# Optimization experiments

Hardware: AMD Instinct MI355X
Metric: run time of the kernel (lower is better)

## Reference

```python
import jax, jax.numpy as jnp
import numpy as np

NUM_HEADS = 16
HIDDEN = 1024
HEAD_DIM = HIDDEN // NUM_HEADS
B, L = 1, 2048


def setup_inputs() -> dict:
    key = jax.random.key(0)
    ks = jax.random.split(key, 5)
    scale = 1.0 / np.sqrt(HIDDEN)
    x = jax.random.normal(ks[0], (B, L, HIDDEN), dtype=jnp.float32)
    Wq = jax.random.normal(ks[1], (HIDDEN, HIDDEN), dtype=jnp.float32) * scale
    Wk = jax.random.normal(ks[2], (HIDDEN, HIDDEN), dtype=jnp.float32) * scale
    Wv = jax.random.normal(ks[3], (HIDDEN, HIDDEN), dtype=jnp.float32) * scale
    Wo = jax.random.normal(ks[4], (HIDDEN, HIDDEN), dtype=jnp.float32) * scale
    return {"x": x, "Wq": Wq, "Wk": Wk, "Wv": Wv, "Wo": Wo}


def reference(x, Wq, Wk, Wv, Wo):
    Bx, Lx, _ = x.shape
    # nn.Linear computes x @ W.T (bias=False)
    q = (x @ Wq.T).reshape(Bx, Lx, NUM_HEADS, HEAD_DIM)
    k = (x @ Wk.T).reshape(Bx, Lx, NUM_HEADS, HEAD_DIM)
    v = (x @ Wv.T).reshape(Bx, Lx, NUM_HEADS, HEAD_DIM)
    # elu(.)+1 feature map
    q = jax.nn.elu(q) + 1.0
    k = jax.nn.elu(k) + 1.0
    # causal linear-attention state via cumsum of kv outer products
    kv = jnp.einsum('blhd,blhe->blhde', k, v)           # [B,L,H,D,D]
    kv_cumsum = jnp.cumsum(kv, axis=1)
    k_cumsum = jnp.cumsum(k, axis=1)
    out = jnp.einsum('blhd,blhde->blhe', q, kv_cumsum)   # [B,L,H,D]
    denom = jnp.clip(jnp.einsum('blhd,blhd->blh', q, k_cumsum), 1e-6, None)
    out = out / denom[..., None]
    return out.reshape(Bx, Lx, HIDDEN) @ Wo.T
```

## Files before the change

kernel.cpp:

```cpp
#include <hip/hip_runtime.h>
#include <hip/hip_bf16.h>

typedef __attribute__((ext_vector_type(8))) short short8;
typedef __attribute__((ext_vector_type(4))) float floatx4;
typedef __attribute__((ext_vector_type(8))) unsigned short ushortx8;
typedef __attribute__((ext_vector_type(4))) unsigned short ushortx4;
typedef unsigned short u16;

#define HIDDEN 1024
#define NH 16
#define HD 64
#define SEQ 2048
#define CHUNK 128
#define NCHUNK (SEQ / CHUNK)

__device__ __forceinline__ u16 f2bf(float f) {
    union { float f; unsigned u; } v; v.f = f;
    unsigned r = v.u + 0x7fffu + ((v.u >> 16) & 1u);
    return (u16)(r >> 16);
}
__device__ __forceinline__ float bf2f(u16 u) {
    union { unsigned u; float f; } v; v.u = ((unsigned)u) << 16;
    return v.f;
}

__device__ __forceinline__ void gl_lds16(const u16* g, u16* l) {
    __builtin_amdgcn_global_load_lds(
        (const __attribute__((address_space(1))) void*)g,
        (__attribute__((address_space(3))) void*)l,
        16, 0, 0);
}

__global__ __launch_bounds__(256)
void convert_all(const float* __restrict__ x,  const float* __restrict__ Wq,
                 const float* __restrict__ Wk, const float* __restrict__ Wv,
                 const float* __restrict__ Wo,
                 u16* __restrict__ xb, u16* __restrict__ Wb, u16* __restrict__ Wob)
{
    const int total4 = 1572864;
    for (int idx = blockIdx.x * 256 + threadIdx.x; idx < total4; idx += gridDim.x * 256) {
        const float4* src; u16* dst; int off;
        if (idx < 524288)       { src = (const float4*)x;  dst = xb;            off = idx; }
        else if (idx < 786432)  { src = (const float4*)Wq; dst = Wb;            off = idx - 524288; }
        else if (idx < 1048576) { src = (const float4*)Wk; dst = Wb + 1048576;  off = idx - 786432; }
        else if (idx < 1310720) { src = (const float4*)Wv; dst = Wb + 2097152;  off = idx - 1048576; }
        else                    { src = (const float4*)Wo; dst = Wob;           off = idx - 1310720; }
        float4 v = src[off];
        ushortx4 u = { f2bf(v.x), f2bf(v.y), f2bf(v.z), f2bf(v.w) };
        *(ushortx4*)(dst + (size_t)off * 4) = u;
    }
}

__global__ __launch_bounds__(256, 3)
void qkv_gemm64(const u16* __restrict__ A, const u16* __restrict__ Bm,
                u16* __restrict__ qkb, u16* __restrict__ kT_b, u16* __restrict__ vT_b)
{
    __shared__ u16 As[2][64 * 64];
    __shared__ u16 Bs[2][128 * 64];
    const int n0 = blockIdx.x * 128, m0 = blockIdx.y * 64;
    const int t = threadIdx.x;
    const int lane = t & 63, wave = t >> 6;
    const int ln = lane & 15, q4 = lane >> 4;
    const int wm = (wave >> 1) * 32, wn = (wave & 1) * 64;
    const int r_in = t >> 3;
    const int csw = (((t & 7) ^ (r_in & 7)) << 3);

    const u16* Ag = A + (size_t)(m0 + r_in) * 1024 + csw;
    const u16* Bg = Bm + (size_t)(n0 + r_in) * 1024 + csw;

    floatx4 acc[2][4];
#pragma unroll
    for (int i = 0; i < 2; i++)
#pragma unroll
        for (int j = 0; j < 4; j++) acc[i][j] = (floatx4)0.0f;

    auto stage = [&](int buf, int k) {
        const int k0 = k * 64;
        gl_lds16(Ag + k0, &As[buf][t * 8]);
        gl_lds16(Ag + k0 + 32 * 1024, &As[buf][2048 + t * 8]);
#pragma unroll
        for (int i = 0; i < 4; i++)
            gl_lds16(Bg + k0 + (size_t)i * 32 * 1024, &Bs[buf][i * 2048 + t * 8]);
    };
    auto compute = [&](int buf) {
#pragma unroll
        for (int s = 0; s < 2; s++) {
            const int rc = (((s * 4 + q4) ^ (ln & 7)) << 3);
            short8 af[2], bfr[4];
#pragma unroll
            for (int i = 0; i < 2; i++)
                af[i] = *(const short8*)&As[buf][(wm + i * 16 + ln) * 64 + rc];
#pragma unroll
            for (int j = 0; j < 4; j++)
                bfr[j] = *(const short8*)&Bs[buf][(wn + j * 16 + ln) * 64 + rc];
#pragma unroll
            for (int i = 0; i < 2; i++)
#pragma unroll
                for (int j = 0; j < 4; j++)
                    acc[i][j] = __builtin_amdgcn_mfma_f32_16x16x32_bf16(af[i], bfr[j], acc[i][j], 0, 0, 0);
        }
    };

    stage(0, 0);
    stage(1, 1);
    for (int i = 0; i < 14; i++) {
        asm volatile("s_waitcnt vmcnt(6)" ::: "memory");
        __builtin_amdgcn_sched_barrier(0);
        __builtin_amdgcn_s_barrier();
        compute(i & 1);
        __builtin_amdgcn_sched_barrier(0);
        __builtin_amdgcn_s_barrier();
        stage(i & 1, i + 2);
    }
    asm volatile("s_waitcnt vmcnt(6)" ::: "memory");
    __builtin_amdgcn_sched_barrier(0);
    __builtin_amdgcn_s_barrier();
    compute(0);
    asm volatile("s_waitcnt vmcnt(0)" ::: "memory");
    __builtin_amdgcn_sched_barrier(0);
    __builtin_amdgcn_s_barrier();
    compute(1);

    const int grp = n0 >> 10;
#pragma unroll
    for (int i = 0; i < 2; i++)
#pragma unroll
        for (int j = 0; j < 4; j++) {
            const int mb = m0 + wm + i * 16 + q4 * 4;
            const int n = n0 + wn + j * 16 + ln;
            const int nh = n & 1023, h = nh >> 6, e = nh & 63;
            float vals[4];
#pragma unroll
            for (int r = 0; r < 4; r++) {
                float v = acc[i][j][r];
                if (grp < 2) v = (v > 0.f) ? (v + 1.f) : __expf(v);
                vals[r] = v;
            }
            if (grp == 0) {
#pragma unroll
                for (int r = 0; r < 4; r++) qkb[(size_t)(mb + r) * 2048 + nh] = f2bf(vals[r]);
            } else if (grp == 1) {
#pragma unroll
                for (int r = 0; r < 4; r++) qkb[(size_t)(mb + r) * 2048 + 1024 + nh] = f2bf(vals[r]);
                ushortx4 u = { f2bf(vals[0]), f2bf(vals[1]), f2bf(vals[2]), f2bf(vals[3]) };
                *(ushortx4*)&kT_b[(size_t)(h * 64 + e) * 2048 + mb] = u;
            } else {
                ushortx4 u = { f2bf(vals[0]), f2bf(vals[1]), f2bf(vals[2]), f2bf(vals[3]) };
                *(ushortx4*)&vT_b[(size_t)(h * 64 + e) * 2048 + mb] = u;
            }
        }
}

__global__ __launch_bounds__(256, 2)
void chunk_stats2(const u16* __restrict__ kT_b, const u16* __restrict__ vT_b,
                  float* __restrict__ S_ws, float* __restrict__ ksum_ws)
{
    __shared__ u16 kT_l[64 * 128];
    __shared__ u16 vT_l[64 * 128];
    const int c = blockIdx.x, h = blockIdx.y;
    const int t = threadIdx.x;
    const int lane = t & 63, w = t >> 6;
    const int ln = lane & 15, q4 = lane >> 4;
#pragma unroll
    for (int i = 0; i < 4; i++) {
        const int d0 = w * 16 + i * 4 + (lane >> 4);
        const int cc = lane & 15;
        const size_t gsrc = (size_t)(h * 64 + d0) * 2048 + c * 128 + ((cc ^ (d0 & 7)) << 3);
        gl_lds16(kT_b + gsrc, &kT_l[(w * 16 + i * 4) * 128 + lane * 8]);
        gl_lds16(vT_b + gsrc, &vT_l[(w * 16 + i * 4) * 128 + lane * 8]);
    }
    __syncthreads();
    floatx4 sacc[4];
#pragma unroll
    for (int j = 0; j < 4; j++) sacc[j] = (floatx4)0.0f;
#pragma unroll
    for (int ks = 0; ks < 4; ks++) {
        const int rc = (((ks * 4 + q4) ^ (ln & 7)) << 3);
        short8 af = *(const short8*)&kT_l[(w * 16 + ln) * 128 + rc];
#pragma unroll
        for (int j = 0; j < 4; j++) {
            short8 bfr = *(const short8*)&vT_l[(j * 16 + ln) * 128 + rc];
            sacc[j] = __builtin_amdgcn_mfma_f32_16x16x32_bf16(af, bfr, sacc[j], 0, 0, 0);
        }
    }
    float* Sp = S_ws + ((size_t)(h * NCHUNK + c) << 12);
#pragma unroll
    for (int j = 0; j < 4; j++)
#pragma unroll
        for (int r = 0; r < 4; r++) {
            int d = w * 16 + q4 * 4 + r;
            int e = j * 16 + ln;
            Sp[e * 64 + d] = sacc[j][r];
        }
    if (t < 64) {
        float s = 0.f;
#pragma unroll
        for (int cc = 0; cc < 16; cc++) {
            ushortx8 v8 = *(const ushortx8*)&kT_l[t * 128 + cc * 8];
#pragma unroll
            for (int jj = 0; jj < 8; jj++) s += bf2f(v8[jj]);
        }
        ksum_ws[(h * NCHUNK + c) * 64 + t] = s;
    }
}

__global__ __launch_bounds__(256)
void scan_kv(const float* __restrict__ S_ws, const float* __restrict__ ksum_ws,
             u16* __restrict__ kvpref_b, float* __restrict__ kspref)
{
    const int h = blockIdx.x, qt = blockIdx.y;
    const int t = threadIdx.x;
    const int li = qt * 1024 + t * 4;
    const int e = li >> 6, d0 = li & 63;
    const int slot = e * 64 + ((((d0 >> 3) ^ (e & 7)) << 3) | (d0 & 7));
    float a0 = 0.f, a1 = 0.f, a2 = 0.f, a3 = 0.f;
    for (int c = 0; c < 16; c++) {
        ushortx4 u = { f2bf(a0), f2bf(a1), f2bf(a2), f2bf(a3) };
        *(ushortx4*)&kvpref_b[(((size_t)(h * 16 + c)) << 12) + slot] = u;
        float4 s4 = *(const float4*)(S_ws + (((size_t)(h * 16 + c)) << 12) + li);
        a0 += s4.x; a1 += s4.y; a2 += s4.z; a3 += s4.w;
    }
    if (qt == 0 && t < 64) {
        float a = 0.f;
        for (int c = 0; c < 16; c++) {
            kspref[(h * 16 + c) * 64 + t] = a;
            a += ksum_ws[(h * 16 + c) * 64 + t];
        }
    }
}

__global__ __launch_bounds__(512, 2)
void attn_out2(const u16* __restrict__ qkb, const u16* __restrict__ vT_b,
               const u16* __restrict__ kvpref_b, const float* __restrict__ kspref,
               u16* __restrict__ attnb)
{
    __shared__ __align__(16) u16 smem[29824];
    u16* q_l   = smem;
    u16* k_l   = smem + 8192;
    u16* kvT_l = smem + 16384;
    u16* vT_l  = smem + 20480;
    u16* P_l   = smem;
    float* kpref  = (float*)(smem + 28672);
    float* denom4 = kpref + 64;

    const int c = blockIdx.x, h = blockIdx.y;
    const int t = threadIdx.x;
    const int lane = t & 63, w = t >> 6;
    const int ln = lane & 15, q4 = lane >> 4;

    {
        const int row = t >> 3, cc = t & 7;
        const size_t gq = (size_t)(c * CHUNK + row) * 2048 + h * 64
                        + (size_t)((cc ^ (row & 7)) << 3);
        gl_lds16(qkb + gq,        &q_l[t * 8]);
        gl_lds16(qkb + gq + 1024, &k_l[t * 8]);
        const int row2 = row + 64;
        const size_t gq2 = (size_t)(c * CHUNK + row2) * 2048 + h * 64
                         + (size_t)((cc ^ (row2 & 7)) << 3);
        gl_lds16(qkb + gq2,        &q_l[4096 + t * 8]);
        gl_lds16(qkb + gq2 + 1024, &k_l[4096 + t * 8]);
        const int d = t >> 4, cv = t & 15;
        gl_lds16(vT_b + (size_t)(h * 64 + d) * 2048 + c * 128 + ((cv ^ (d & 7)) << 3),
                 &vT_l[t * 8]);
        const int d2 = d + 32;
        gl_lds16(vT_b + (size_t)(h * 64 + d2) * 2048 + c * 128 + ((cv ^ (d2 & 7)) << 3),
                 &vT_l[4096 + t * 8]);
        gl_lds16(kvpref_b + (((size_t)(h * 16 + c)) << 12) + t * 8, &kvT_l[t * 8]);
    }
    if (t < 64) kpref[t] = kspref[(h * 16 + c) * 64 + t];
    __syncthreads();

    const int pm = (w >> 2) * 64, pn = (w & 3) * 32;
    floatx4 pacc[4][2];
#pragma unroll
    for (int i = 0; i < 4; i++)
#pragma unroll
        for (int j = 0; j < 2; j++) pacc[i][j] = (floatx4)0.0f;
#pragma unroll
    for (int s = 0; s < 2; s++) {
        const int rc = (((s * 4 + q4) ^ (ln & 7)) << 3);
        short8 af[4], bfr[2];
#pragma unroll
        for (int i = 0; i < 4; i++)
            af[i] = *(const short8*)&q_l[(pm + i * 16 + ln) * 64 + rc];
#pragma unroll
        for (int j = 0; j < 2; j++)
            bfr[j] = *(const short8*)&k_l[(pn + j * 16 + ln) * 64 + rc];
#pragma unroll
        for (int i = 0; i < 4; i++)
#pragma unroll
            for (int j = 0; j < 2; j++)
                pacc[i][j] = __builtin_amdgcn_mfma_f32_16x16x32_bf16(af[i], bfr[j], pacc[i][j], 0, 0, 0);
    }
#pragma unroll
    for (int i = 0; i < 4; i++)
#pragma unroll
        for (int r = 0; r < 4; r++) {
            int rowi = pm + i * 16 + q4 * 4 + r;
            float rs = 0.f;
#pragma unroll
            for (int j = 0; j < 2; j++) {
                int col = pn + j * 16 + ln;
                float p = pacc[i][j][r];
                if (col > rowi) p = 0.f;
                pacc[i][j][r] = p;
                rs += p;
            }
#pragma unroll
            for (int off = 1; off < 16; off <<= 1) rs += __shfl_xor(rs, off, 64);
            if (ln == 0) denom4[(w & 3) * 128 + rowi] = rs;
        }
    const int ob = w * 16;
    floatx4 oacc[4];
#pragma unroll
    for (int j = 0; j < 4; j++) oacc[j] = (floatx4)0.0f;
#pragma unroll
    for (int s = 0; s < 2; s++) {
        const int rc = (((s * 4 + q4) ^ (ln & 7)) << 3);
        short8 af = *(const short8*)&q_l[(ob + ln) * 64 + rc];
#pragma unroll
        for (int j = 0; j < 4; j++) {
            short8 bfr = *(const short8*)&kvT_l[(j * 16 + ln) * 64 + rc];
            oacc[j] = __builtin_amdgcn_mfma_f32_16x16x32_bf16(af, bfr, oacc[j], 0, 0, 0);
        }
    }
    __syncthreads();
    if (t < 128) {
        float s = 0.f;
#pragma unroll
        for (int c8 = 0; c8 < 8; c8++) {
            ushortx8 v8 = *(const ushortx8*)&q_l[t * 64 + ((c8 ^ (t & 7)) << 3)];
#pragma unroll
            for (int jj = 0; jj < 8; jj++) s += bf2f(v8[jj]) * kpref[c8 * 8 + jj];
        }
        denom4[t] += s;
    }
    __syncthreads();
#pragma unroll
    for (int i = 0; i < 4; i++)
#pragma unroll
        for (int j = 0; j < 2; j++)
#pragma unroll
            for (int r = 0; r < 4; r++) {
                int rowi = pm + i * 16 + q4 * 4 + r;
                int col = pn + j * 16 + ln;
                P_l[rowi * 136 + col] = f2bf(pacc[i][j][r]);
            }
    __syncthreads();
    for (int ks = 0; ks <= (w >> 1); ks++) {
        short8 af = *(const short8*)&P_l[(ob + ln) * 136 + ks * 32 + q4 * 8];
        const int rc = (((ks * 4 + q4) ^ (ln & 7)) << 3);
#pragma unroll
        for (int j = 0; j < 4; j++) {
            short8 bfr = *(const short8*)&vT_l[(j * 16 + ln) * 128 + rc];
            oacc[j] = __builtin_amdgcn_mfma_f32_16x16x32_bf16(af, bfr, oacc[j], 0, 0, 0);
        }
    }
#pragma unroll
    for (int r = 0; r < 4; r++) {
        const int rowi = ob + q4 * 4 + r;
        float den = denom4[rowi] + denom4[128 + rowi] + denom4[256 + rowi] + denom4[384 + rowi];
        den = fmaxf(den, 1e-6f);
#pragma unroll
        for (int j = 0; j < 4; j++) {
            int e = j * 16 + ln;
            attnb[(size_t)(c * CHUNK + rowi) * HIDDEN + h * HD + e] = f2bf(oacc[j][r] / den);
        }
    }
}

__global__ __launch_bounds__(256, 3)
void out_gemm64(const u16* __restrict__ A, const u16* __restrict__ Bm,
                float* __restrict__ out)
{
    __shared__ u16 As[2][64 * 64];
    __shared__ u16 Bs[2][64 * 64];
    const int n0 = blockIdx.x * 64, m0 = blockIdx.y * 64;
    const int t = threadIdx.x;
    const int lane = t & 63, wave = t >> 6;
    const int ln = lane & 15, q4 = lane >> 4;
    const int wm = (wave >> 1) * 32, wn = (wave & 1) * 32;
    const int r_in = t >> 3;
    const int csw = (((t & 7) ^ (r_in & 7)) << 3);

    const u16* Ag = A + (size_t)(m0 + r_in) * 1024 + csw;
    const u16* Bg = Bm + (size_t)(n0 + r_in) * 1024 + csw;

    floatx4 acc[2][2];
#pragma unroll
    for (int i = 0; i < 2; i++)
#pragma unroll
        for (int j = 0; j < 2; j++) acc[i][j] = (floatx4)0.0f;

    auto stage = [&](int buf, int k) {
        const int k0 = k * 64;
        gl_lds16(Ag + k0, &As[buf][t * 8]);
        gl_lds16(Ag + k0 + 32 * 1024, &As[buf][2048 + t * 8]);
        gl_lds16(Bg + k0, &Bs[buf][t * 8]);
        gl_lds16(Bg + k0 + 32 * 1024, &Bs[buf][2048 + t * 8]);
    };
    auto compute = [&](int buf) {
#pragma unroll
        for (int s = 0; s < 2; s++) {
            const int rc = (((s * 4 + q4) ^ (ln & 7)) << 3);
            short8 af[2], bfr[2];
#pragma unroll
            for (int i = 0; i < 2; i++)
                af[i] = *(const short8*)&As[buf][(wm + i * 16 + ln) * 64 + rc];
#pragma unroll
            for (int j = 0; j < 2; j++)
                bfr[j] = *(const short8*)&Bs[buf][(wn + j * 16 + ln) * 64 + rc];
#pragma unroll
            for (int i = 0; i < 2; i++)
#pragma unroll
                for (int j = 0; j < 2; j++)
                    acc[i][j] = __builtin_amdgcn_mfma_f32_16x16x32_bf16(af[i], bfr[j], acc[i][j], 0, 0, 0);
        }
    };

    stage(0, 0);
    stage(1, 1);
    for (int i = 0; i < 14; i++) {
        asm volatile("s_waitcnt vmcnt(4)" ::: "memory");
        __builtin_amdgcn_sched_barrier(0);
        __builtin_amdgcn_s_barrier();
        compute(i & 1);
        __builtin_amdgcn_sched_barrier(0);
        __builtin_amdgcn_s_barrier();
        stage(i & 1, i + 2);
    }
    asm volatile("s_waitcnt vmcnt(4)" ::: "memory");
    __builtin_amdgcn_sched_barrier(0);
    __builtin_amdgcn_s_barrier();
    compute(0);
    asm volatile("s_waitcnt vmcnt(0)" ::: "memory");
    __builtin_amdgcn_sched_barrier(0);
    __builtin_amdgcn_s_barrier();
    compute(1);

#pragma unroll
    for (int i = 0; i < 2; i++)
#pragma unroll
        for (int j = 0; j < 2; j++)
#pragma unroll
            for (int r = 0; r < 4; r++) {
                int m = m0 + wm + i * 16 + q4 * 4 + r;
                int n = n0 + wn + j * 16 + ln;
                out[(size_t)m * 1024 + n] = acc[i][j][r];
            }
}

extern "C" void kernel_launch(void* const* d_in, const int* in_sizes, int n_in,
                              void* d_out, int out_size, void* d_ws, size_t ws_size,
                              hipStream_t stream)
{
    const float* x  = (const float*)d_in[0];
    const float* Wq = (const float*)d_in[1];
    const float* Wk = (const float*)d_in[2];
    const float* Wv = (const float*)d_in[3];
    const float* Wo = (const float*)d_in[4];
    float* out = (float*)d_out;

    char* ws = (char*)d_ws;
    const size_t MB = 1024 * 1024;
    u16* xb    = (u16*)(ws);
    u16* Wb    = (u16*)(ws + 4 * MB);
    u16* Wob   = (u16*)(ws + 10 * MB);
    u16* qkb   = (u16*)(ws + 12 * MB);
    u16* kT_b  = (u16*)(ws + 20 * MB);
    u16* vT_b  = (u16*)(ws + 24 * MB);
    float* S_ws    = (float*)(ws + 28 * MB);
    float* ksum_ws = (float*)(ws + 32 * MB);
    u16* attnb = (u16*)(ws + 33 * MB);
    u16* kvpref_b = (u16*)(ws + 37 * MB);
    float* kspref = (float*)(ws + 39 * MB);

    convert_all<<<2048, 256, 0, stream>>>(x, Wq, Wk, Wv, Wo, xb, Wb, Wob);
    qkv_gemm64<<<dim3(24, 32), 256, 0, stream>>>(xb, Wb, qkb, kT_b, vT_b);
    chunk_stats2<<<dim3(NCHUNK, NH), 256, 0, stream>>>(kT_b, vT_b, S_ws, ksum_ws);
    scan_kv<<<dim3(NH, 4), 256, 0, stream>>>(S_ws, ksum_ws, kvpref_b, kspref);
    attn_out2<<<dim3(NCHUNK, NH), 512, 0, stream>>>(qkb, vT_b, kvpref_b, kspref, attnb);
    out_gemm64<<<dim3(16, 32), 256, 0, stream>>>(attnb, Wob, out);
}
```

Baseline: 124.2 us.

## Stage QKV GEMM epilogue through LDS and remap block tiles for cache locality

The QKV GEMM epilogue now writes results into shared memory, one row-major and one transposed tile, and then emits 16-byte coalesced stores to qkb, kT_b and vT_b. Before, it issued scattered 2-byte and 8-byte global stores. Both GEMMs also switch to a 1D grid whose block indices are remapped into groups, presumably to spread tiles across the XCDs and improve L2 reuse of A and B tiles. This adds an extra LDS round trip and two barriers at the end of each block.

Result: slower. 127.8 us (+2.9%).

```diff
diff --git a/kernel.cpp b/kernel.cpp
--- a/kernel.cpp
+++ b/kernel.cpp
@@ -55,9 +55,17 @@
 void qkv_gemm64(const u16* __restrict__ A, const u16* __restrict__ Bm,
                 u16* __restrict__ qkb, u16* __restrict__ kT_b, u16* __restrict__ vT_b)
 {
-    __shared__ u16 As[2][64 * 64];
-    __shared__ u16 Bs[2][128 * 64];
-    const int n0 = blockIdx.x * 128, m0 = blockIdx.y * 64;
+    __shared__ __align__(16) u16 smem[24576];
+    auto As = (u16(*)[4096])smem;
+    auto Bs = (u16(*)[8192])(smem + 8192);
+    u16* Trow = smem;
+    u16* Tcol = smem + 8704;
+
+    const int L = blockIdx.x;
+    const int xc = L & 7, i5 = L >> 3;
+    const int m0 = (((xc >> 2) * 16) + (i5 & 15)) * 64;
+    const int n0 = (((xc & 3) * 6) + (i5 >> 4)) * 128;
+
     const int t = threadIdx.x;
     const int lane = t & 63, wave = t >> 6;
     const int ln = lane & 15, q4 = lane >> 4;
@@ -121,14 +129,14 @@
     __builtin_amdgcn_s_barrier();
     compute(1);
 
+    __syncthreads();
     const int grp = n0 >> 10;
 #pragma unroll
     for (int i = 0; i < 2; i++)
 #pragma unroll
         for (int j = 0; j < 4; j++) {
-            const int mb = m0 + wm + i * 16 + q4 * 4;
-            const int n = n0 + wn + j * 16 + ln;
-            const int nh = n & 1023, h = nh >> 6, e = nh & 63;
+            const int ml = wm + i * 16 + q4 * 4;
+            const int nl = wn + j * 16 + ln;
             float vals[4];
 #pragma unroll
             for (int r = 0; r < 4; r++) {
@@ -136,19 +144,35 @@
                 if (grp < 2) v = (v > 0.f) ? (v + 1.f) : __expf(v);
                 vals[r] = v;
             }
-            if (grp == 0) {
-#pragma unroll
-                for (int r = 0; r < 4; r++) qkb[(size_t)(mb + r) * 2048 + nh] = f2bf(vals[r]);
-            } else if (grp == 1) {
-#pragma unroll
-                for (int r = 0; r < 4; r++) qkb[(size_t)(mb + r) * 2048 + 1024 + nh] = f2bf(vals[r]);
+            if (grp < 2) {
+#pragma unroll
+                for (int r = 0; r < 4; r++) Trow[(ml + r) * 136 + nl] = f2bf(vals[r]);
+            }
+            if (grp >= 1) {
                 ushortx4 u = { f2bf(vals[0]), f2bf(vals[1]), f2bf(vals[2]), f2bf(vals[3]) };
-                *(ushortx4*)&kT_b[(size_t)(h * 64 + e) * 2048 + mb] = u;
-            } else {
-                ushortx4 u = { f2bf(vals[0]), f2bf(vals[1]), f2bf(vals[2]), f2bf(vals[3]) };
-                *(ushortx4*)&vT_b[(size_t)(h * 64 + e) * 2048 + mb] = u;
+                *(ushortx4*)&Tcol[nl * 72 + ml] = u;
             }
         }
+    __syncthreads();
+    if (grp < 2) {
+        const int ml = t >> 2, sg = (t & 3) * 32;
+        const int col0 = (n0 & 1023) + (grp ? 1024 : 0) + sg;
+        const u16* src = &Trow[ml * 136 + sg];
+        u16* dst = &qkb[(size_t)(m0 + ml) * 2048 + col0];
+#pragma unroll
+        for (int p = 0; p < 4; p++)
+            *(ushortx8*)&dst[p * 8] = *(const ushortx8*)&src[p * 8];
+    }
+    if (grp >= 1) {
+        const int nl = t >> 1, sg = (t & 1) * 32;
+        const int nh = (n0 & 1023) + nl;
+        const u16* src = &Tcol[nl * 72 + sg];
+        u16* dstb = (grp == 1) ? kT_b : vT_b;
+        u16* dst = &dstb[(size_t)nh * 2048 + m0 + sg];
+#pragma unroll
+        for (int p = 0; p < 4; p++)
+            *(ushortx8*)&dst[p * 8] = *(const ushortx8*)&src[p * 8];
+    }
 }
 
 __global__ __launch_bounds__(256, 2)
@@ -375,7 +399,10 @@
 {
     __shared__ u16 As[2][64 * 64];
     __shared__ u16 Bs[2][64 * 64];
-    const int n0 = blockIdx.x * 64, m0 = blockIdx.y * 64;
+    const int L = blockIdx.x;
+    const int xc = L & 7, i6 = L >> 3;
+    const int m0 = (((xc >> 1) * 8) + (i6 & 7)) * 64;
+    const int n0 = (((xc & 1) * 8) + (i6 >> 3)) * 64;
     const int t = threadIdx.x;
     const int lane = t & 63, wave = t >> 6;
     const int ln = lane & 15, q4 = lane >> 4;
@@ -476,9 +503,9 @@
     float* kspref = (float*)(ws + 39 * MB);
 
     convert_all<<<2048, 256, 0, stream>>>(x, Wq, Wk, Wv, Wo, xb, Wb, Wob);
-    qkv_gemm64<<<dim3(24, 32), 256, 0, stream>>>(xb, Wb, qkb, kT_b, vT_b);
+    qkv_gemm64<<<768, 256, 0, stream>>>(xb, Wb, qkb, kT_b, vT_b);
     chunk_stats2<<<dim3(NCHUNK, NH), 256, 0, stream>>>(kT_b, vT_b, S_ws, ksum_ws);
     scan_kv<<<dim3(NH, 4), 256, 0, stream>>>(S_ws, ksum_ws, kvpref_b, kspref);
     attn_out2<<<dim3(NCHUNK, NH), 512, 0, stream>>>(qkb, vT_b, kvpref_b, kspref, attnb);
-    out_gemm64<<<dim3(16, 32), 256, 0, stream>>>(attnb, Wob, out);
-}
+    out_gemm64<<<512, 256, 0, stream>>>(attnb, Wob, out);
+}
```
